# Kernel tuning notes

Hardware: AMD Instinct MI355X
Metric: run time of the kernel (lower is better)

Reference implementation:

```python
import jax, jax.numpy as jnp
import numpy as np

N_NODES = 100000
N_EDGES = 1600000
IN_FEATS = 128
OUT_FEATS = 48


def setup_inputs() -> dict:
    key = jax.random.key(0)
    ks = jax.random.split(key, 6)
    features = jax.random.normal(ks[0], (N_NODES, IN_FEATS), dtype=jnp.float32)
    # xavier_uniform for W.weight [out, in]
    lim_w = float(np.sqrt(6.0 / (IN_FEATS + OUT_FEATS)))
    W_w = jax.random.uniform(ks[1], (OUT_FEATS, IN_FEATS), dtype=jnp.float32, minval=-lim_w, maxval=lim_w)
    W_b = jnp.zeros((OUT_FEATS,), dtype=jnp.float32)
    # xavier_uniform for attn_w [2*out, 1]
    lim_a = float(np.sqrt(6.0 / (2 * OUT_FEATS + 1)))
    attn_w = jax.random.uniform(ks[2], (2 * OUT_FEATS, 1), dtype=jnp.float32, minval=-lim_a, maxval=lim_a)
    attn_b = jnp.zeros((1,), dtype=jnp.float32)
    src = jax.random.randint(ks[3], (N_EDGES,), 0, N_NODES, dtype=jnp.int32)
    dst = jax.random.randint(ks[4], (N_EDGES,), 0, N_NODES, dtype=jnp.int32)
    return {"features": features, "W_w": W_w, "W_b": W_b,
            "attn_w": attn_w, "attn_b": attn_b, "src": src, "dst": dst}


def reference(features, W_w, W_b, attn_w, attn_b, src, dst):
    n = features.shape[0]
    d = W_w.shape[0]
    # h = W(features)  [N, d]
    h = features @ W_w.T + W_b
    # cat([h[src], h[dst]]) @ attn_w == h[src] @ w_src + h[dst] @ w_dst
    w_src = attn_w[:d, 0]   # [d]
    w_dst = attn_w[d:, 0]   # [d]
    s_src = h @ w_src       # [N]
    s_dst = h @ w_dst       # [N]
    e = s_src[src] + s_dst[dst] + attn_b[0]            # [E]
    e = jax.nn.leaky_relu(e, negative_slope=0.2)
    # edge softmax grouped by destination node
    m = jax.ops.segment_max(e, dst, num_segments=n)     # [N]
    ex = jnp.exp(e - m[dst])                            # [E]
    denom = jax.ops.segment_sum(ex, dst, num_segments=n)  # [N]
    alpha = ex / denom[dst]                             # [E]
    # weighted scatter-sum: out[v] = sum_{(u,v) in E} alpha * h[u]
    msgs = h[src] * alpha[:, None]                      # [E, d]
    out = jax.ops.segment_sum(msgs, dst, num_segments=n)  # [N, d]
    return out
```

## Files before the change

kernel.cpp:

```cpp
#include <hip/hip_runtime.h>

#define NFEAT 128
#define DOUT 48
#define BSH 6
#define BNODES 64
#define PCAP 192
#define BCAP (PCAP * 8)
#define EPT 16
#define NBMAX 1568
#define HSTRIDE 32

typedef __attribute__((ext_vector_type(8))) short bf16x8;
typedef __attribute__((ext_vector_type(4))) float f32x4;

__device__ __forceinline__ float bf_lo(unsigned u) { return __uint_as_float(u << 16); }
__device__ __forceinline__ float bf_hi(unsigned u) { return __uint_as_float(u & 0xFFFF0000u); }
__device__ __forceinline__ unsigned bf_pack(float a, float b) {
    unsigned ua = __float_as_uint(a), ub = __float_as_uint(b);
    ua = (ua + 0x7FFFu + ((ua >> 16) & 1u)) >> 16;
    ub = (ub + 0x7FFFu + ((ub >> 16) & 1u)) & 0xFFFF0000u;
    return ua | ub;
}

__device__ __forceinline__ void split2(float x, short& hi, short& lo) {
    unsigned u = __float_as_uint(x);
    unsigned h = u & 0xFFFF0000u;
    hi = (short)(h >> 16);
    float r = x - __uint_as_float(h);
    unsigned v = __float_as_uint(r);
    lo = (short)((v + 0x7FFFu + ((v >> 16) & 1u)) >> 16);
}

__global__ __launch_bounds__(256) void k_proj(
    const float* __restrict__ feat, const float* __restrict__ Ww,
    const float* __restrict__ Wb, const float* __restrict__ attn_w,
    unsigned* __restrict__ hbf, float* __restrict__ s_src, float* __restrict__ s_dst,
    int n)
{
    __shared__ float hb[128][49];

    int tid  = threadIdx.x;
    int lane = tid & 63;
    int wv   = tid >> 6;
    int g    = lane >> 4;
    int r16  = lane & 15;

    int mbase = blockIdx.x * 128 + wv * 32;
    int na0 = mbase + r16;       if (na0 >= n) na0 = n - 1;
    int na1 = mbase + 16 + r16;  if (na1 >= n) na1 = n - 1;

    const float* fA0 = feat + (size_t)na0 * NFEAT + g * 4;
    const float* fA1 = feat + (size_t)na1 * NFEAT + g * 4;
    const float* wB  = Ww + (size_t)r16 * NFEAT + g * 4;

    f32x4 acc[2][3];
#pragma unroll
    for (int mt = 0; mt < 2; ++mt)
#pragma unroll
        for (int nt = 0; nt < 3; ++nt)
            acc[mt][nt] = (f32x4){0.f, 0.f, 0.f, 0.f};

#pragma unroll
    for (int ks = 0; ks < 4; ++ks) {
        f32x4 ra[4], rb[6];
        ra[0] = *(const f32x4*)(fA0 + ks * 32);
        ra[1] = *(const f32x4*)(fA0 + ks * 32 + 16);
        ra[2] = *(const f32x4*)(fA1 + ks * 32);
        ra[3] = *(const f32x4*)(fA1 + ks * 32 + 16);
        rb[0] = *(const f32x4*)(wB + ks * 32);
        rb[1] = *(const f32x4*)(wB + ks * 32 + 16);
        rb[2] = *(const f32x4*)(wB + 16 * NFEAT + ks * 32);
        rb[3] = *(const f32x4*)(wB + 16 * NFEAT + ks * 32 + 16);
        rb[4] = *(const f32x4*)(wB + 32 * NFEAT + ks * 32);
        rb[5] = *(const f32x4*)(wB + 32 * NFEAT + ks * 32 + 16);

        bf16x8 Ah[2], Al[2], Bh[3], Bl[3];
#pragma unroll
        for (int t = 0; t < 2; ++t) {
#pragma unroll
            for (int i = 0; i < 4; ++i) {
                short h, l;
                split2(ra[2 * t][i], h, l);     Ah[t][i] = h;     Al[t][i] = l;
                split2(ra[2 * t + 1][i], h, l); Ah[t][i + 4] = h; Al[t][i + 4] = l;
            }
        }
#pragma unroll
        for (int t = 0; t < 3; ++t) {
#pragma unroll
            for (int i = 0; i < 4; ++i) {
                short h, l;
                split2(rb[2 * t][i], h, l);     Bh[t][i] = h;     Bl[t][i] = l;
                split2(rb[2 * t + 1][i], h, l); Bh[t][i + 4] = h; Bl[t][i + 4] = l;
            }
        }
#pragma unroll
        for (int mt = 0; mt < 2; ++mt)
#pragma unroll
            for (int nt = 0; nt < 3; ++nt) {
                acc[mt][nt] = __builtin_amdgcn_mfma_f32_16x16x32_bf16(Ah[mt], Bh[nt], acc[mt][nt], 0, 0, 0);
                acc[mt][nt] = __builtin_amdgcn_mfma_f32_16x16x32_bf16(Al[mt], Bh[nt], acc[mt][nt], 0, 0, 0);
                acc[mt][nt] = __builtin_amdgcn_mfma_f32_16x16x32_bf16(Ah[mt], Bl[nt], acc[mt][nt], 0, 0, 0);
            }
    }

#pragma unroll
    for (int mt = 0; mt < 2; ++mt)
#pragma unroll
        for (int nt = 0; nt < 3; ++nt)
#pragma unroll
            for (int rr = 0; rr < 4; ++rr)
                hb[wv * 32 + mt * 16 + 4 * g + rr][nt * 16 + r16] = acc[mt][nt][rr];
    __syncthreads();

    int node = tid >> 1, part = tid & 1, jb = part * 24;
    int gn = blockIdx.x * 128 + node;
    float v[24];
    float ss = 0.f, sd = 0.f;
#pragma unroll
    for (int j = 0; j < 24; ++j) {
        float x = hb[node][jb + j] + Wb[jb + j];
        v[j] = x;
        ss = fmaf(x, attn_w[jb + j], ss);
        sd = fmaf(x, attn_w[DOUT + jb + j], sd);
    }
    ss += __shfl_xor(ss, 1, 64);
    sd += __shfl_xor(sd, 1, 64);

    if (gn < n) {
#pragma unroll
        for (int q = 0; q < 4; ++q) {
            int sub = part * 4 + q;
            uint4 u;
            u.x = bf_pack(v[6 * q + 0], v[6 * q + 1]);
            u.y = bf_pack(v[6 * q + 2], v[6 * q + 3]);
            u.z = bf_pack(v[6 * q + 4], v[6 * q + 5]);
            u.w = 0;
            *(uint4*)(hbf + (size_t)gn * HSTRIDE + sub * 4) = u;
        }
        if (part == 0) {
            s_src[gn] = ss;
            s_dst[gn] = sd;
        }
    }
}

__global__ __launch_bounds__(256) void k_bin(
    const int4* __restrict__ src4, const int4* __restrict__ dst4,
    const float* __restrict__ s_src, const float* __restrict__ s_dst,
    const float* __restrict__ attn_b,
    int* __restrict__ cursor, int2* __restrict__ ents, int nE, int NB)
{
    __shared__ int hist[NBMAX];
    __shared__ int bas[NBMAX];

    int tid = threadIdx.x;
    int cls = blockIdx.x & 7;
    long long e0 = (long long)blockIdx.x * 4096 + (long long)tid * EPT;

    for (int t = tid; t < NB; t += 256) hist[t] = 0;
    __syncthreads();

    int s[EPT], d[EPT];
    bool any = (e0 < nE);
#pragma unroll
    for (int q = 0; q < EPT / 4; ++q) {
        int4 sv = any ? src4[e0 / 4 + q] : make_int4(0, 0, 0, 0);
        int4 dv = any ? dst4[e0 / 4 + q] : make_int4(0, 0, 0, 0);
        s[4 * q + 0] = sv.x; s[4 * q + 1] = sv.y; s[4 * q + 2] = sv.z; s[4 * q + 3] = sv.w;
        d[4 * q + 0] = dv.x; d[4 * q + 1] = dv.y; d[4 * q + 2] = dv.z; d[4 * q + 3] = dv.w;
    }

    float vs[EPT], vd[EPT];
#pragma unroll
    for (int u = 0; u < EPT; ++u) vs[u] = s_src[s[u]];
#pragma unroll
    for (int u = 0; u < EPT; ++u) vd[u] = s_dst[d[u]];

    int rank[EPT];
#pragma unroll
    for (int u = 0; u < EPT; ++u)
        rank[u] = (e0 + u < nE) ? atomicAdd(&hist[d[u] >> BSH], 1) : 0;
    __syncthreads();

    for (int t = tid; t < NB; t += 256) {
        int c = hist[t];
        if (c > 0) bas[t] = atomicAdd(cursor + cls * NB + t, c);
    }
    __syncthreads();

    float ab = attn_b[0];
#pragma unroll
    for (int u = 0; u < EPT; ++u) {
        if (e0 + u < nE) {
            float v = vs[u] + vd[u] + ab;
            v = (v > 0.f) ? v : 0.2f * v;
            float x = __expf(v);
            int bkt = d[u] >> BSH;
            int slot = bas[bkt] + rank[u];
            if (slot < PCAP)
                ents[(size_t)bkt * BCAP + cls * PCAP + slot] =
                    make_int2(s[u] | ((d[u] & (BNODES - 1)) << 17), __float_as_int(x));
        }
    }
}

__global__ __launch_bounds__(256) void k_aggb(
    const unsigned* __restrict__ hbf, const int* __restrict__ cursor,
    const int2* __restrict__ ents, float* __restrict__ out, int n, int NB)
{
    __shared__ int2 sse[BCAP];
    __shared__ int c1[BNODES], c2[BNODES], lrp[BNODES + 1];
    __shared__ int cp[9];

    int b = blockIdx.x;
    int tid = threadIdx.x;
    const int2* ebase = ents + (size_t)b * BCAP;

    if (tid < BNODES) { c1[tid] = 0; c2[tid] = 0; }
    if (tid < 8) {
        int c = min(cursor[tid * NB + b], PCAP);
        int p = c;
#pragma unroll
        for (int o = 1; o < 8; o <<= 1) {
            int u = __shfl_up(p, o, 64);
            if (tid >= o) p += u;
        }
        cp[tid + 1] = p;
        if (tid == 0) cp[0] = 0;
    }
    __syncthreads();
    int total = cp[8];

    for (int i = tid; i < total; i += 256) {
        int c = 0;
        while (i >= cp[c + 1]) ++c;
        int x = ebase[c * PCAP + (i - cp[c])].x;
        atomicAdd(&c1[((unsigned)x) >> 17], 1);
    }
    __syncthreads();

    if (tid < BNODES) {
        int v = c1[tid];
        int p = v;
#pragma unroll
        for (int o = 1; o < 64; o <<= 1) {
            int u = __shfl_up(p, o, 64);
            if (tid >= o) p += u;
        }
        lrp[tid] = p - v;
        if (tid == BNODES - 1) lrp[BNODES] = p;
    }
    __syncthreads();

    for (int i = tid; i < total; i += 256) {
        int c = 0;
        while (i >= cp[c + 1]) ++c;
        int2 v = ebase[c * PCAP + (i - cp[c])];
        int dl = ((unsigned)v.x) >> 17;
        int pos = lrp[dl] + atomicAdd(&c2[dl], 1);
        sse[pos] = v;
    }
    __syncthreads();

    int wave = tid >> 6, lane = tid & 63;
    int g = lane >> 3, sub = lane & 7;
    for (int dl = wave; dl < BNODES; dl += 4) {
        int node = (b << BSH) + dl;
        if (node >= n) break;
        int st = lrp[dl], en = lrp[dl + 1];
        float a0 = 0.f, a1 = 0.f, a2 = 0.f, a3 = 0.f, a4 = 0.f, a5 = 0.f, den = 0.f;
        int k = st + g;
        for (; k + 8 < en; k += 16) {
            int2 e1 = sse[k];
            int2 e2 = sse[k + 8];
            uint4 h1 = *(const uint4*)(hbf + (size_t)(e1.x & 0x1FFFF) * HSTRIDE + sub * 4);
            uint4 h2 = *(const uint4*)(hbf + (size_t)(e2.x & 0x1FFFF) * HSTRIDE + sub * 4);
            float x1 = __int_as_float(e1.y), x2 = __int_as_float(e2.y);
            den += x1; den += x2;
            a0 = fmaf(x1, bf_lo(h1.x), a0);
            a1 = fmaf(x1, bf_hi(h1.x), a1);
            a2 = fmaf(x1, bf_lo(h1.y), a2);
            a3 = fmaf(x1, bf_hi(h1.y), a3);
            a4 = fmaf(x1, bf_lo(h1.z), a4);
            a5 = fmaf(x1, bf_hi(h1.z), a5);
            a0 = fmaf(x2, bf_lo(h2.x), a0);
            a1 = fmaf(x2, bf_hi(h2.x), a1);
            a2 = fmaf(x2, bf_lo(h2.y), a2);
            a3 = fmaf(x2, bf_hi(h2.y), a3);
            a4 = fmaf(x2, bf_lo(h2.z), a4);
            a5 = fmaf(x2, bf_hi(h2.z), a5);
        }
        if (k < en) {
            int2 ed = sse[k];
            float x = __int_as_float(ed.y);
            den += x;
            uint4 h0 = *(const uint4*)(hbf + (size_t)(ed.x & 0x1FFFF) * HSTRIDE + sub * 4);
            a0 = fmaf(x, bf_lo(h0.x), a0);
            a1 = fmaf(x, bf_hi(h0.x), a1);
            a2 = fmaf(x, bf_lo(h0.y), a2);
            a3 = fmaf(x, bf_hi(h0.y), a3);
            a4 = fmaf(x, bf_lo(h0.z), a4);
            a5 = fmaf(x, bf_hi(h0.z), a5);
        }
#pragma unroll
        for (int o = 8; o <= 32; o <<= 1) {
            a0  += __shfl_xor(a0, o, 64);
            a1  += __shfl_xor(a1, o, 64);
            a2  += __shfl_xor(a2, o, 64);
            a3  += __shfl_xor(a3, o, 64);
            a4  += __shfl_xor(a4, o, 64);
            a5  += __shfl_xor(a5, o, 64);
            den += __shfl_xor(den, o, 64);
        }
        if (lane < 8) {
            float inv = (en > st) ? 1.f / den : 0.f;
            float* op = out + (size_t)node * DOUT + sub * 6;
            op[0] = a0 * inv;
            op[1] = a1 * inv;
            op[2] = a2 * inv;
            op[3] = a3 * inv;
            op[4] = a4 * inv;
            op[5] = a5 * inv;
        }
    }
}

extern "C" void kernel_launch(void* const* d_in, const int* in_sizes, int n_in,
                              void* d_out, int out_size, void* d_ws, size_t ws_size,
                              hipStream_t stream) {
    const float* feat   = (const float*)d_in[0];
    const float* Ww     = (const float*)d_in[1];
    const float* Wb     = (const float*)d_in[2];
    const float* attn_w = (const float*)d_in[3];
    const float* attn_b = (const float*)d_in[4];
    const int*   src    = (const int*)d_in[5];
    const int*   dst    = (const int*)d_in[6];

    int n  = in_sizes[0] / NFEAT;
    int nE = in_sizes[5];
    int NB = (n + BNODES - 1) / BNODES;
    int N8 = NB * 8;
    float* out = (float*)d_out;

    unsigned* hbf  = (unsigned*)d_ws;
    float* s_src   = (float*)(hbf + (size_t)n * HSTRIDE);
    float* s_dst   = s_src + n;
    int*   cursor  = (int*)(s_dst + n);
    int2*  ents    = (int2*)(cursor + N8);

    hipMemsetAsync(cursor, 0, (size_t)N8 * sizeof(int), stream);

    int NBp = (n + 127) / 128;
    k_proj<<<NBp, 256, 0, stream>>>(feat, Ww, Wb, attn_w, hbf, s_src, s_dst, n);
    int nbb = (nE + 4095) / 4096;
    k_bin<<<nbb, 256, 0, stream>>>((const int4*)src, (const int4*)dst,
                                   s_src, s_dst, attn_b, cursor, ents, nE, NB);
    k_aggb<<<NB, 256, 0, stream>>>(hbf, cursor, ents, out, n, NB);
}
```

Measured before the change: 190.4 us.

## Stage bucket entries in LDS once and give each node an 8-lane group

Bucket entries are now read from global memory once and staged into a shared-memory array while counting, so the second scatter pass reads from LDS instead of re-reading global memory with a per-element chunk search. The aggregation mapping changes from one wave per destination node, which needed cross-lane shuffle reductions, to one 8-lane group per node. Each group walks that node's edges serially, two at a time, with no reduction step. This removes the shuffle reductions and idle lanes on low-degree nodes. In exchange it doubles shared-memory use, which may lower occupancy, and each group's gather loop is serial and uneven across nodes.

```diff
diff --git a/kernel.cpp b/kernel.cpp
--- a/kernel.cpp
+++ b/kernel.cpp
@@ -208,6 +208,7 @@
     const unsigned* __restrict__ hbf, const int* __restrict__ cursor,
     const int2* __restrict__ ents, float* __restrict__ out, int n, int NB)
 {
+    __shared__ int2 se[BCAP];
     __shared__ int2 sse[BCAP];
     __shared__ int c1[BNODES], c2[BNODES], lrp[BNODES + 1];
     __shared__ int cp[9];
@@ -231,11 +232,14 @@
     __syncthreads();
     int total = cp[8];
 
-    for (int i = tid; i < total; i += 256) {
-        int c = 0;
-        while (i >= cp[c + 1]) ++c;
-        int x = ebase[c * PCAP + (i - cp[c])].x;
-        atomicAdd(&c1[((unsigned)x) >> 17], 1);
+#pragma unroll
+    for (int c = 0; c < 8; ++c) {
+        int s0 = cp[c], s1 = cp[c + 1];
+        for (int i = s0 + tid; i < s1; i += 256) {
+            int2 v = ebase[c * PCAP + (i - s0)];
+            se[i] = v;
+            atomicAdd(&c1[((unsigned)v.x) >> 17], 1);
+        }
     }
     __syncthreads();
 
@@ -253,26 +257,27 @@
     __syncthreads();
 
     for (int i = tid; i < total; i += 256) {
-        int c = 0;
-        while (i >= cp[c + 1]) ++c;
-        int2 v = ebase[c * PCAP + (i - cp[c])];
+        int2 v = se[i];
         int dl = ((unsigned)v.x) >> 17;
         int pos = lrp[dl] + atomicAdd(&c2[dl], 1);
         sse[pos] = v;
     }
     __syncthreads();
 
-    int wave = tid >> 6, lane = tid & 63;
-    int g = lane >> 3, sub = lane & 7;
-    for (int dl = wave; dl < BNODES; dl += 4) {
+    int grp = tid >> 3;
+    int sub = tid & 7;
+#pragma unroll
+    for (int pass = 0; pass < 2; ++pass) {
+        int dl = grp + pass * 32;
         int node = (b << BSH) + dl;
-        if (node >= n) break;
-        int st = lrp[dl], en = lrp[dl + 1];
+        bool live = (node < n);
+        int st = lrp[dl];
+        int en = live ? lrp[dl + 1] : st;
         float a0 = 0.f, a1 = 0.f, a2 = 0.f, a3 = 0.f, a4 = 0.f, a5 = 0.f, den = 0.f;
-        int k = st + g;
-        for (; k + 8 < en; k += 16) {
+        int k = st;
+        for (; k + 1 < en; k += 2) {
             int2 e1 = sse[k];
-            int2 e2 = sse[k + 8];
+            int2 e2 = sse[k + 1];
             uint4 h1 = *(const uint4*)(hbf + (size_t)(e1.x & 0x1FFFF) * HSTRIDE + sub * 4);
             uint4 h2 = *(const uint4*)(hbf + (size_t)(e2.x & 0x1FFFF) * HSTRIDE + sub * 4);
             float x1 = __int_as_float(e1.y), x2 = __int_as_float(e2.y);
@@ -302,17 +307,7 @@
             a4 = fmaf(x, bf_lo(h0.z), a4);
             a5 = fmaf(x, bf_hi(h0.z), a5);
         }
-#pragma unroll
-        for (int o = 8; o <= 32; o <<= 1) {
-            a0  += __shfl_xor(a0, o, 64);
-            a1  += __shfl_xor(a1, o, 64);
-            a2  += __shfl_xor(a2, o, 64);
-            a3  += __shfl_xor(a3, o, 64);
-            a4  += __shfl_xor(a4, o, 64);
-            a5  += __shfl_xor(a5, o, 64);
-            den += __shfl_xor(den, o, 64);
-        }
-        if (lane < 8) {
+        if (live) {
             float inv = (en > st) ? 1.f / den : 0.f;
             float* op = out + (size_t)node * DOUT + sub * 6;
             op[0] = a0 * inv;
```

After: 190.8 us. No clear change (+0.2%).
